# Optimization experiments

Measured on AMD Instinct MI355X. Metric: run time of the kernel, lower is better.

The kernel has to match this reference:

```python
import jax, jax.numpy as jnp
import numpy as np

LN_EPS = 1e-6
NEG = -1e9

def setup_inputs() -> dict:
    key = jax.random.key(0)
    k1, k2, k3 = jax.random.split(key, 3)
    B, S, E, H = 4, 2048, 1024, 4
    D = E // H
    x = jax.random.normal(k1, (B, S, E), dtype=jnp.float32)
    qkv_w = jax.random.normal(k2, (3, H, E, D), dtype=jnp.float32) * 0.02
    out_w = jax.random.normal(k3, (E, E), dtype=jnp.float32) * 0.02
    ln_gamma = jnp.ones((E,), dtype=jnp.float32)
    ln_beta = jnp.zeros((E,), dtype=jnp.float32)
    return {"x": x, "qkv_w": qkv_w, "out_w": out_w, "ln_gamma": ln_gamma, "ln_beta": ln_beta}

def reference(x, qkv_w, out_w, ln_gamma, ln_beta):
    B, S, E = x.shape
    H = qkv_w.shape[1]
    q = jnp.einsum('bse,hed->bhsd', x, qkv_w[0])
    k = jnp.einsum('bse,hed->bhsd', x, qkv_w[1])
    v = jnp.einsum('bse,hed->bhsd', x, qkv_w[2])
    # NOTE: original scales by sqrt(embedding_size), NOT sqrt(head_dim).
    scores = jnp.einsum('bhsd,bhtd->bhst', q, k) / jnp.sqrt(jnp.float32(E))
    # look-ahead (causal) mask: 1 above diagonal -> add -1e9
    causal = 1.0 - jnp.tril(jnp.ones((S, S), dtype=scores.dtype))
    scores = scores + causal * NEG
    attn = jax.nn.softmax(scores, axis=-1)
    out = jnp.einsum('bhst,bhtd->bhsd', attn, v)        # [b,h,s,d]
    # concat heads -> [b,s,e]
    out = out.transpose(0, 2, 1, 3).reshape(B, S, E)
    out = out @ out_w
    y = out + x  # residual
    mean = jnp.mean(y, axis=-1, keepdims=True)
    var = jnp.mean(jnp.square(y - mean), axis=-1, keepdims=True)
    return (y - mean) * jax.lax.rsqrt(var + LN_EPS) * ln_gamma + ln_beta
```

## Files before the change

### kernel.cpp

```cpp
#include <hip/hip_runtime.h>

typedef __attribute__((ext_vector_type(8))) __bf16 bf16x8;
typedef __attribute__((ext_vector_type(4))) float f32x4;
typedef __attribute__((ext_vector_type(16))) float f32x16;
typedef unsigned short u16;
typedef unsigned int u32;

#define BB 4
#define SS 2048
#define EE 1024
#define HH 4
#define DD 256

#define GLOAD_LDS(g, l) __builtin_amdgcn_global_load_lds( \
    (const __attribute__((address_space(1))) unsigned int*)(g), \
    (__attribute__((address_space(3))) unsigned int*)(l), 16, 0, 0)

__device__ __forceinline__ u16 f2bf(float f) {
  unsigned int u = __float_as_uint(f);
  u = (u + 0x7FFFu + ((u >> 16) & 1u)) >> 16;
  return (u16)u;
}

__global__ __launch_bounds__(256) void cast_bf16_k(const float* __restrict__ in,
                                                   u16* __restrict__ out, int n4) {
  int i = blockIdx.x * 256 + threadIdx.x;
  if (i >= n4) return;
  float4 v = ((const float4*)in)[i];
  union { u16 s[4]; uint2 u; } o;
  o.s[0] = f2bf(v.x); o.s[1] = f2bf(v.y); o.s[2] = f2bf(v.z); o.s[3] = f2bf(v.w);
  ((uint2*)out)[i] = o.u;
}

__global__ __launch_bounds__(256) void transpose_cast_k(const float* __restrict__ in,
                                                        u16* __restrict__ out, int R, int C,
                                                        float scale_q) {
  __shared__ float tile[32][33];
  size_t moff = (size_t)blockIdx.z * R * C;
  in += moff; out += moff;
  float sc = (blockIdx.z < 4) ? scale_q : 1.0f;
  int c0 = blockIdx.x * 32, r0 = blockIdx.y * 32;
  int tx = threadIdx.x, ty = threadIdx.y;
  #pragma unroll
  for (int i = 0; i < 4; ++i)
    tile[ty + 8*i][tx] = in[(size_t)(r0 + ty + 8*i) * C + c0 + tx];
  __syncthreads();
  #pragma unroll
  for (int i = 0; i < 4; ++i)
    out[(size_t)(c0 + ty + 8*i) * R + r0 + tx] = f2bf(tile[tx][ty + 8*i] * sc);
}

__device__ __forceinline__ void gemm128(const u16* __restrict__ A, int lda,
                                        const u16* __restrict__ Bt, int ldb,
                                        int row0, int col0, int K,
                                        u16* As, u16* Bs, f32x4 acc[4][4]) {
  int t = threadIdx.x;
  int lane = t & 63, w = t >> 6;
  int wr = w >> 1, wc = w & 1;
  int lr = lane & 15, kg = lane >> 4;
  f32x4 z = {0.f, 0.f, 0.f, 0.f};
  #pragma unroll
  for (int m = 0; m < 4; ++m)
    #pragma unroll
    for (int n = 0; n < 4; ++n) acc[m][n] = z;
  for (int kt = 0; kt < K; kt += 64) {
    __syncthreads();
    #pragma unroll
    for (int it = 0; it < 4; ++it) {
      int Lb = it*4096 + w*1024 + lane*16;
      int row = Lb >> 7;
      int scb = ((Lb >> 4) & 7) ^ (row & 7);
      GLOAD_LDS(A  + (size_t)(row0 + row) * lda + kt + scb*8,
                (char*)As + it*4096 + w*1024);
      GLOAD_LDS(Bt + (size_t)(col0 + row) * ldb + kt + scb*8,
                (char*)Bs + it*4096 + w*1024);
    }
    __syncthreads();
    __builtin_amdgcn_s_setprio(1);
    #pragma unroll
    for (int kk = 0; kk < 2; ++kk) {
      bf16x8 af[4], bfr[4];
      #pragma unroll
      for (int m = 0; m < 4; ++m) {
        int row = wr*64 + m*16 + lr;
        int bo = (row << 7) + ((((kk << 6) + (kg << 4))) ^ ((row & 7) << 4));
        af[m] = *(const bf16x8*)((const char*)As + bo);
      }
      #pragma unroll
      for (int n = 0; n < 4; ++n) {
        int row = wc*64 + n*16 + lr;
        int bo = (row << 7) + ((((kk << 6) + (kg << 4))) ^ ((row & 7) << 4));
        bfr[n] = *(const bf16x8*)((const char*)Bs + bo);
      }
      #pragma unroll
      for (int m = 0; m < 4; ++m)
        #pragma unroll
        for (int n = 0; n < 4; ++n)
          acc[m][n] = __builtin_amdgcn_mfma_f32_16x16x32_bf16(af[m], bfr[n], acc[m][n], 0, 0, 0);
    }
    __builtin_amdgcn_s_setprio(0);
  }
}

__global__ __launch_bounds__(256) void qkv_gemm_k(const u16* __restrict__ xb,
                                                  const u16* __restrict__ wt,
                                                  u16* __restrict__ qb,
                                                  u16* __restrict__ kp,
                                                  u16* __restrict__ vp) {
  __shared__ u16 As[128*64], Bs[128*64];
  int bid = blockIdx.x;
  int mh = bid >> 7;
  int tt = bid & 127;
  int mt = tt & 63, nt = tt >> 6;
  f32x4 acc[4][4];
  gemm128(xb, EE, wt + (size_t)mh * DD * EE, EE, mt*128, nt*128, EE, As, Bs, acc);
  int t = threadIdx.x, lane = t & 63, w = t >> 6;
  int wr = w >> 1, wc = w & 1, lr = lane & 15, kg = lane >> 4;
  int qi = mh >> 2, h = mh & 3;
  if (qi == 0) {
    #pragma unroll
    for (int m = 0; m < 4; ++m)
      #pragma unroll
      for (int n = 0; n < 4; ++n)
        #pragma unroll
        for (int j = 0; j < 4; ++j) {
          int r = mt*128 + wr*64 + m*16 + kg*4 + j;
          int c = nt*128 + wc*64 + n*16 + lr;
          int b = r >> 11, s = r & 2047;
          qb[(size_t)((b*HH + h) * SS + s) * DD + c] = f2bf(acc[m][n][j]);
        }
  } else if (qi == 1) {
    #pragma unroll
    for (int m = 0; m < 4; ++m)
      #pragma unroll
      for (int n = 0; n < 4; ++n)
        #pragma unroll
        for (int j = 0; j < 4; ++j) {
          int r = mt*128 + wr*64 + m*16 + kg*4 + j;
          int d = nt*128 + wc*64 + n*16 + lr;
          int b = r >> 11, srow = r & 2047;
          int bh = b*HH + h, c = srow >> 5, l31 = srow & 31;
          int kb = d >> 4, hfd = (d >> 3) & 1, e = d & 7;
          kp[(((size_t)(bh*64 + c)*16 + kb)*64 + hfd*32 + l31)*8 + e] = f2bf(acc[m][n][j]);
        }
  } else {
    int hfs = (kg >> 1) & 1, e0 = (kg & 1) * 4;
    #pragma unroll
    for (int m = 0; m < 4; ++m)
      #pragma unroll
      for (int n = 0; n < 4; ++n) {
        int r = mt*128 + wr*64 + m*16 + kg*4;
        int d = nt*128 + wc*64 + n*16 + lr;
        int b = r >> 11, srow = r & 2047;
        int bh = b*HH + h, c = srow >> 5;
        int kb2 = (srow >> 4) & 1;
        int db = d >> 5, l31 = d & 31;
        union { u16 s4[4]; uint2 u; } pk;
        #pragma unroll
        for (int j = 0; j < 4; ++j) pk.s4[j] = f2bf(acc[m][n][j]);
        *(uint2*)(vp + ((((size_t)(bh*64 + c)*8 + db)*2 + kb2)*64 + hfs*32 + l31)*8 + e0) = pk.u;
      }
  }
}

__global__ __launch_bounds__(512, 2) void attn_k(const u16* __restrict__ Qb,
                                                 const u16* __restrict__ Kp,
                                                 const u16* __restrict__ Vp,
                                                 u16* __restrict__ ctx) {
  int bid = blockIdx.x;
  int xcd = bid & 7;
  int p   = bid >> 3;
  int tid = threadIdx.x, wid = tid >> 6, lane = tid & 63;
  int ks = wid & 3, dh = wid >> 2;
  int l31 = lane & 31, hf = lane >> 5;

  __shared__ float Ob[32 * 256];
  __shared__ float stats[4][32][2];
  __shared__ u16 Qs[16 * 64 * 8];

  for (int bhp = 0; bhp < 2; ++bhp) {
    int bh = xcd + 8 * bhp;
    int b = bh >> 2, h = bh & 3;
    const u16* Q = Qb + (size_t)bh * SS * DD;
    size_t bh64 = (size_t)bh * 64;

    for (int tp = 0; tp < 2; ++tp) {
      int qt = tp ? p : 63 - p;
      int q0 = qt * 32;

      #pragma unroll
      for (int i = 0; i < 2; ++i) {
        int kb = wid*2 + i;
        uint4 qv = *(const uint4*)(Q + (size_t)(q0 + l31) * DD + kb*16 + hf*8);
        *(uint4*)((char*)Qs + kb*1024 + lane*16) = qv;
      }
      __syncthreads();

      f32x16 o[4];
      #pragma unroll
      for (int j = 0; j < 4; ++j)
        #pragma unroll
        for (int r = 0; r < 16; ++r) o[j][r] = 0.f;
      float m = -1e30f, lsum = 0.f;

      int n = qt + 1;
      int c0 = (n * ks) >> 2, c1 = (n * (ks + 1)) >> 2;

      for (int c = c0; c < c1; ++c) {
        const u16* kpc = Kp + (bh64 + c) * (16 * 512);
        const u16* vpc = Vp + (bh64 + c) * (16 * 512);
        bf16x8 vf[8];
        #pragma unroll
        for (int i = 0; i < 8; ++i)
          vf[i] = *(const bf16x8*)(vpc + (dh*8 + i)*512 + lane*8);
        bf16x8 kfa[8];
        #pragma unroll
        for (int kb = 0; kb < 8; ++kb)
          kfa[kb] = *(const bf16x8*)(kpc + kb*512 + lane*8);
        __builtin_amdgcn_sched_barrier(0);

        f32x16 sA, sB;
        #pragma unroll
        for (int r = 0; r < 16; ++r) { sA[r] = 0.f; sB[r] = 0.f; }
        __builtin_amdgcn_s_setprio(1);
        #pragma unroll
        for (int kb = 0; kb < 8; ++kb) {
          bf16x8 qv = *(const bf16x8*)((const char*)Qs + kb*1024 + lane*16);
          sA = __builtin_amdgcn_mfma_f32_32x32x16_bf16(kfa[kb], qv, sA, 0, 0, 0);
          if (kb == 3) __builtin_amdgcn_sched_barrier(0);
        }
        __builtin_amdgcn_s_setprio(0);
        __builtin_amdgcn_sched_barrier(0);
        bf16x8 kfb[8];
        #pragma unroll
        for (int kb = 0; kb < 8; ++kb)
          kfb[kb] = *(const bf16x8*)(kpc + (8 + kb)*512 + lane*8);
        __builtin_amdgcn_sched_barrier(0);
        __builtin_amdgcn_s_setprio(1);
        #pragma unroll
        for (int kb = 0; kb < 8; ++kb) {
          bf16x8 qv = *(const bf16x8*)((const char*)Qs + (8 + kb)*1024 + lane*16);
          sB = __builtin_amdgcn_mfma_f32_32x32x16_bf16(kfb[kb], qv, sB, 0, 0, 0);
          if (kb == 3) __builtin_amdgcn_sched_barrier(0);
        }
        __builtin_amdgcn_s_setprio(0);

        float pr[16];
        #pragma unroll
        for (int r = 0; r < 16; ++r) pr[r] = sA[r] + sB[r];
        if (c == qt) {
          #pragma unroll
          for (int r = 0; r < 16; ++r) {
            int key = (r & 3) + 8*(r >> 2) + 4*hf;
            if (key > l31) pr[r] = -1e9f;
          }
        }
        float mx = pr[0];
        #pragma unroll
        for (int r = 1; r < 16; ++r) mx = fmaxf(mx, pr[r]);
        mx = fmaxf(mx, __shfl_xor(mx, 32));
        if (!__all(mx <= m + 11.5f)) {
          float mnew = fmaxf(m, mx);
          float al = exp2f(m - mnew);
          lsum *= al;
          #pragma unroll
          for (int j = 0; j < 4; ++j) o[j] *= al;
          m = mnew;
        }
        float psum = 0.f;
        #pragma unroll
        for (int r = 0; r < 16; ++r) { pr[r] = exp2f(pr[r] - m); psum += pr[r]; }
        psum += __shfl_xor(psum, 32);
        lsum += psum;
        u32 cpk[8];
        #pragma unroll
        for (int i = 0; i < 8; ++i) {
          u32 rpk;
          asm("v_cvt_pk_bf16_f32 %0, %1, %2" : "=v"(rpk) : "v"(pr[2*i]), "v"(pr[2*i+1]));
          cpk[i] = rpk;
        }
        u32 x0 = (u32)__shfl_xor((int)(hf ? cpk[0] : cpk[2]), 32);
        u32 x1 = (u32)__shfl_xor((int)(hf ? cpk[1] : cpk[3]), 32);
        u32 x2 = (u32)__shfl_xor((int)(hf ? cpk[4] : cpk[6]), 32);
        u32 x3 = (u32)__shfl_xor((int)(hf ? cpk[5] : cpk[7]), 32);
        union { u32 w[4]; bf16x8 v; } pb0, pb1;
        pb0.w[0] = hf ? x0 : cpk[0];
        pb0.w[1] = hf ? x1 : cpk[1];
        pb0.w[2] = hf ? cpk[2] : x0;
        pb0.w[3] = hf ? cpk[3] : x1;
        pb1.w[0] = hf ? x2 : cpk[4];
        pb1.w[1] = hf ? x3 : cpk[5];
        pb1.w[2] = hf ? cpk[6] : x2;
        pb1.w[3] = hf ? cpk[7] : x3;
        __builtin_amdgcn_s_setprio(1);
        #pragma unroll
        for (int j = 0; j < 4; ++j) {
          o[j] = __builtin_amdgcn_mfma_f32_32x32x16_bf16(vf[j*2+0], pb0.v, o[j], 0, 0, 0);
          o[j] = __builtin_amdgcn_mfma_f32_32x32x16_bf16(vf[j*2+1], pb1.v, o[j], 0, 0, 0);
        }
        __builtin_amdgcn_s_setprio(0);
      }

      __syncthreads();
      if (lane < 32 && wid < 4) { stats[wid][l31][0] = m; stats[wid][l31][1] = lsum; }
      __syncthreads();
      float mg = fmaxf(fmaxf(stats[0][l31][0], stats[1][l31][0]),
                       fmaxf(stats[2][l31][0], stats[3][l31][0]));
      float beta = exp2f(m - mg);
      #pragma unroll
      for (int j = 0; j < 4; ++j) o[j] *= beta;

      #pragma unroll
      for (int tau = 0; tau < 4; ++tau) {
        int jr = (ks + tau) & 3;
        f32x16 osel = (jr == 0) ? o[0] : (jr == 1) ? o[1] : (jr == 2) ? o[2] : o[3];
        #pragma unroll
        for (int u = 0; u < 4; ++u) {
          int byteoff = l31*1024 + ((((dh*4 + jr)*128) + u*32 + hf*16) ^ ((l31 & 7) << 4));
          float* ptr = (float*)((char*)Ob + byteoff);
          f32x4 val = { osel[4*u+0], osel[4*u+1], osel[4*u+2], osel[4*u+3] };
          if (tau == 0) *(f32x4*)ptr = val;
          else {
            f32x4 old = *(f32x4*)ptr;
            *(f32x4*)ptr = old + val;
          }
        }
        __syncthreads();
      }

      if (tid < 256) {
        int q = tid >> 3, dg = tid & 7;
        float mgq = fmaxf(fmaxf(stats[0][q][0], stats[1][q][0]),
                          fmaxf(stats[2][q][0], stats[3][q][0]));
        float lg = exp2f(stats[0][q][0] - mgq) * stats[0][q][1]
                 + exp2f(stats[1][q][0] - mgq) * stats[1][q][1]
                 + exp2f(stats[2][q][0] - mgq) * stats[2][q][1]
                 + exp2f(stats[3][q][0] - mgq) * stats[3][q][1];
        float linv = 1.f / lg;
        u16* crow = ctx + (size_t)(b*SS + q0 + q) * EE + h*DD + dg*32;
        union { u16 s16[16]; uint4 u4[2]; } outp;
        #pragma unroll
        for (int i = 0; i < 8; ++i) {
          int byteoff = q*1024 + ((dg*128 + i*16) ^ ((q & 7) << 4));
          f32x4 v = *(const f32x4*)((const char*)Ob + byteoff);
          #pragma unroll
          for (int j = 0; j < 4; ++j) outp.s16[(i*4+j) & 15] = f2bf(v[j] * linv);
          if (i == 3) {
            *(uint4*)(crow + 0) = outp.u4[0];
            *(uint4*)(crow + 8) = outp.u4[1];
          }
          if (i == 7) {
            *(uint4*)(crow + 16) = outp.u4[0];
            *(uint4*)(crow + 24) = outp.u4[1];
          }
        }
      }
      __syncthreads();
    }
  }
}

__global__ __launch_bounds__(256) void proj_gemm_k(const u16* __restrict__ ctx,
                                                   const u16* __restrict__ wot,
                                                   const float* __restrict__ x,
                                                   float* __restrict__ y) {
  __shared__ u16 As[128*64], Bs[128*64];
  int bid = blockIdx.x;
  int mt = bid & 63, nt = bid >> 6;
  f32x4 acc[4][4];
  gemm128(ctx, EE, wot, EE, mt*128, nt*128, EE, As, Bs, acc);
  int t = threadIdx.x, lane = t & 63, w = t >> 6;
  int wr = w >> 1, wc = w & 1, lr = lane & 15, kg = lane >> 4;
  #pragma unroll
  for (int m = 0; m < 4; ++m)
    #pragma unroll
    for (int n = 0; n < 4; ++n)
      #pragma unroll
      for (int j = 0; j < 4; ++j) {
        int r = mt*128 + wr*64 + m*16 + kg*4 + j;
        int c = nt*128 + wc*64 + n*16 + lr;
        size_t idx = (size_t)r * EE + c;
        y[idx] = acc[m][n][j] + x[idx];
      }
}

__global__ __launch_bounds__(256) void ln_k(float* __restrict__ y,
                                            const float* __restrict__ gamma,
                                            const float* __restrict__ beta) {
  int row = blockIdx.x;
  int t = threadIdx.x;
  float4 v = *((const float4*)(y + (size_t)row * EE) + t);
  float s = v.x + v.y + v.z + v.w;
  float ss = v.x*v.x + v.y*v.y + v.z*v.z + v.w*v.w;
  #pragma unroll
  for (int off = 1; off < 64; off <<= 1) {
    s  += __shfl_xor(s, off);
    ss += __shfl_xor(ss, off);
  }
  __shared__ float rs[4], rss[4];
  int w = t >> 6, lane = t & 63;
  if (lane == 0) { rs[w] = s; rss[w] = ss; }
  __syncthreads();
  s  = rs[0] + rs[1] + rs[2] + rs[3];
  ss = rss[0] + rss[1] + rss[2] + rss[3];
  float mean = s * (1.f / EE);
  float var  = ss * (1.f / EE) - mean * mean;
  float rstd = rsqrtf(var + 1e-6f);
  float4 g  = *((const float4*)gamma + t);
  float4 be = *((const float4*)beta + t);
  float4 ov;
  ov.x = (v.x - mean) * rstd * g.x + be.x;
  ov.y = (v.y - mean) * rstd * g.y + be.y;
  ov.z = (v.z - mean) * rstd * g.z + be.z;
  ov.w = (v.w - mean) * rstd * g.w + be.w;
  *((float4*)(y + (size_t)row * EE) + t) = ov;
}

extern "C" void kernel_launch(void* const* d_in, const int* in_sizes, int n_in,
                              void* d_out, int out_size, void* d_ws, size_t ws_size,
                              hipStream_t stream) {
  const float* x      = (const float*)d_in[0];
  const float* qkv_w  = (const float*)d_in[1];
  const float* out_w  = (const float*)d_in[2];
  const float* gamma  = (const float*)d_in[3];
  const float* beta   = (const float*)d_in[4];
  float* out = (float*)d_out;
  char* ws = (char*)d_ws;

  u16* xb  = (u16*)(ws);
  u16* ctx = xb;
  u16* wqt = (u16*)(ws + 16777216);
  u16* wot = (u16*)(ws + 23068672);
  u16* Qb  = (u16*)(ws + 25165824);
  u16* Kpb = Qb + (size_t)BB*HH*SS*DD;
  u16* Vpb = Kpb + (size_t)BB*HH*SS*DD;

  const float QSC = 0.03125f * 1.44269504088896340736f;

  cast_bf16_k<<<8192, 256, 0, stream>>>(x, xb, (BB*SS*EE)/4);
  transpose_cast_k<<<dim3(8, 32, 12), dim3(32, 8), 0, stream>>>(qkv_w, wqt, EE, DD, QSC);
  transpose_cast_k<<<dim3(32, 32, 1), dim3(32, 8), 0, stream>>>(out_w, wot, EE, EE, 1.0f);
  qkv_gemm_k<<<1536, 256, 0, stream>>>(xb, wqt, Qb, Kpb, Vpb);
  attn_k<<<256, 512, 0, stream>>>(Qb, Kpb, Vpb, ctx);
  proj_gemm_k<<<512, 256, 0, stream>>>(ctx, wot, x, out);
  ln_k<<<8192, 256, 0, stream>>>(out, gamma, beta);
}
```

Before: 202.0 us.

## Double-buffer K/V register fragments to prefetch next attention chunk

Measured after the change: 304.3 us. 50.6% more time.

```diff
diff --git a/kernel.cpp b/kernel.cpp
--- a/kernel.cpp
+++ b/kernel.cpp
@@ -155,12 +155,115 @@
         int bh = b*HH + h, c = srow >> 5;
         int kb2 = (srow >> 4) & 1;
         int db = d >> 5, l31 = d & 31;
-        union { u16 s4[4]; uint2 u; } pk;
+        union { u16 s4[4]; uint2 u2; } pk;
         #pragma unroll
         for (int j = 0; j < 4; ++j) pk.s4[j] = f2bf(acc[m][n][j]);
-        *(uint2*)(vp + ((((size_t)(bh*64 + c)*8 + db)*2 + kb2)*64 + hfs*32 + l31)*8 + e0) = pk.u;
-      }
-  }
+        *(uint2*)(vp + ((((size_t)(bh*64 + c)*8 + db)*2 + kb2)*64 + hfs*32 + l31)*8 + e0) = pk.u2;
+      }
+  }
+}
+
+__device__ __forceinline__ void attn_chunk(
+    int c, int qt, int c1,
+    const u16* __restrict__ Kp0, const u16* __restrict__ Vp0,
+    int dh, int l31, int hf, int lane, const char* Qs,
+    bf16x8 (&kc)[8], bf16x8 (&vc)[8],
+    bf16x8 (&kn)[8], bf16x8 (&vn)[8],
+    f32x16 (&o)[4], float& m, float& lsum) {
+  const u16* kpc = Kp0 + (size_t)c * (16 * 512);
+  bf16x8 kfb[8];
+  #pragma unroll
+  for (int kb = 0; kb < 8; ++kb)
+    kfb[kb] = *(const bf16x8*)(kpc + (8 + kb)*512 + lane*8);
+  __builtin_amdgcn_sched_barrier(0);
+
+  f32x16 sA, sB;
+  #pragma unroll
+  for (int r = 0; r < 16; ++r) { sA[r] = 0.f; sB[r] = 0.f; }
+  __builtin_amdgcn_s_setprio(1);
+  #pragma unroll
+  for (int kb = 0; kb < 8; ++kb) {
+    bf16x8 qv = *(const bf16x8*)(Qs + kb*1024 + lane*16);
+    sA = __builtin_amdgcn_mfma_f32_32x32x16_bf16(kc[kb], qv, sA, 0, 0, 0);
+    if (kb == 3) __builtin_amdgcn_sched_barrier(0);
+  }
+  __builtin_amdgcn_s_setprio(0);
+  __builtin_amdgcn_sched_barrier(0);
+  __builtin_amdgcn_s_setprio(1);
+  #pragma unroll
+  for (int kb = 0; kb < 8; ++kb) {
+    bf16x8 qv = *(const bf16x8*)(Qs + (8 + kb)*1024 + lane*16);
+    sB = __builtin_amdgcn_mfma_f32_32x32x16_bf16(kfb[kb], qv, sB, 0, 0, 0);
+    if (kb == 3) __builtin_amdgcn_sched_barrier(0);
+  }
+  __builtin_amdgcn_s_setprio(0);
+
+  float pr[16];
+  #pragma unroll
+  for (int r = 0; r < 16; ++r) pr[r] = sA[r] + sB[r];
+  if (c == qt) {
+    #pragma unroll
+    for (int r = 0; r < 16; ++r) {
+      int key = (r & 3) + 8*(r >> 2) + 4*hf;
+      if (key > l31) pr[r] = -1e9f;
+    }
+  }
+  float mx = pr[0];
+  #pragma unroll
+  for (int r = 1; r < 16; ++r) mx = fmaxf(mx, pr[r]);
+  mx = fmaxf(mx, __shfl_xor(mx, 32));
+  if (!__all(mx <= m + 11.5f)) {
+    float mnew = fmaxf(m, mx);
+    float al = exp2f(m - mnew);
+    lsum *= al;
+    #pragma unroll
+    for (int j = 0; j < 4; ++j) o[j] *= al;
+    m = mnew;
+  }
+  float psum = 0.f;
+  #pragma unroll
+  for (int r = 0; r < 16; ++r) { pr[r] = exp2f(pr[r] - m); psum += pr[r]; }
+  psum += __shfl_xor(psum, 32);
+  lsum += psum;
+
+  if (c + 1 < c1) {
+    const u16* kpn = Kp0 + (size_t)(c + 1) * (16 * 512);
+    const u16* vpn = Vp0 + (size_t)(c + 1) * (16 * 512);
+    #pragma unroll
+    for (int i = 0; i < 8; ++i)
+      vn[i] = *(const bf16x8*)(vpn + (dh*8 + i)*512 + lane*8);
+    #pragma unroll
+    for (int kb = 0; kb < 8; ++kb)
+      kn[kb] = *(const bf16x8*)(kpn + kb*512 + lane*8);
+  }
+
+  u32 cpk[8];
+  #pragma unroll
+  for (int i = 0; i < 8; ++i) {
+    u32 rpk;
+    asm("v_cvt_pk_bf16_f32 %0, %1, %2" : "=v"(rpk) : "v"(pr[2*i]), "v"(pr[2*i+1]));
+    cpk[i] = rpk;
+  }
+  u32 x0 = (u32)__shfl_xor((int)(hf ? cpk[0] : cpk[2]), 32);
+  u32 x1 = (u32)__shfl_xor((int)(hf ? cpk[1] : cpk[3]), 32);
+  u32 x2 = (u32)__shfl_xor((int)(hf ? cpk[4] : cpk[6]), 32);
+  u32 x3 = (u32)__shfl_xor((int)(hf ? cpk[5] : cpk[7]), 32);
+  union { u32 w[4]; bf16x8 v; } pb0, pb1;
+  pb0.w[0] = hf ? x0 : cpk[0];
+  pb0.w[1] = hf ? x1 : cpk[1];
+  pb0.w[2] = hf ? cpk[2] : x0;
+  pb0.w[3] = hf ? cpk[3] : x1;
+  pb1.w[0] = hf ? x2 : cpk[4];
+  pb1.w[1] = hf ? x3 : cpk[5];
+  pb1.w[2] = hf ? cpk[6] : x2;
+  pb1.w[3] = hf ? cpk[7] : x3;
+  __builtin_amdgcn_s_setprio(1);
+  #pragma unroll
+  for (int j = 0; j < 4; ++j) {
+    o[j] = __builtin_amdgcn_mfma_f32_32x32x16_bf16(vc[j*2+0], pb0.v, o[j], 0, 0, 0);
+    o[j] = __builtin_amdgcn_mfma_f32_32x32x16_bf16(vc[j*2+1], pb1.v, o[j], 0, 0, 0);
+  }
+  __builtin_amdgcn_s_setprio(0);
 }
 
 __global__ __launch_bounds__(512, 2) void attn_k(const u16* __restrict__ Qb,
@@ -182,7 +285,8 @@
     int bh = xcd + 8 * bhp;
     int b = bh >> 2, h = bh & 3;
     const u16* Q = Qb + (size_t)bh * SS * DD;
-    size_t bh64 = (size_t)bh * 64;
+    const u16* Kp0 = Kp + (size_t)bh * 64 * (16 * 512);
+    const u16* Vp0 = Vp + (size_t)bh * 64 * (16 * 512);
 
     for (int tp = 0; tp < 2; ++tp) {
       int qt = tp ? p : 63 - p;
@@ -206,99 +310,27 @@
       int n = qt + 1;
       int c0 = (n * ks) >> 2, c1 = (n * (ks + 1)) >> 2;
 
-      for (int c = c0; c < c1; ++c) {
-        const u16* kpc = Kp + (bh64 + c) * (16 * 512);
-        const u16* vpc = Vp + (bh64 + c) * (16 * 512);
-        bf16x8 vf[8];
-        #pragma unroll
-        for (int i = 0; i < 8; ++i)
-          vf[i] = *(const bf16x8*)(vpc + (dh*8 + i)*512 + lane*8);
-        bf16x8 kfa[8];
-        #pragma unroll
-        for (int kb = 0; kb < 8; ++kb)
-          kfa[kb] = *(const bf16x8*)(kpc + kb*512 + lane*8);
-        __builtin_amdgcn_sched_barrier(0);
-
-        f32x16 sA, sB;
-        #pragma unroll
-        for (int r = 0; r < 16; ++r) { sA[r] = 0.f; sB[r] = 0.f; }
-        __builtin_amdgcn_s_setprio(1);
-        #pragma unroll
-        for (int kb = 0; kb < 8; ++kb) {
-          bf16x8 qv = *(const bf16x8*)((const char*)Qs + kb*1024 + lane*16);
-          sA = __builtin_amdgcn_mfma_f32_32x32x16_bf16(kfa[kb], qv, sA, 0, 0, 0);
-          if (kb == 3) __builtin_amdgcn_sched_barrier(0);
-        }
-        __builtin_amdgcn_s_setprio(0);
-        __builtin_amdgcn_sched_barrier(0);
-        bf16x8 kfb[8];
-        #pragma unroll
-        for (int kb = 0; kb < 8; ++kb)
-          kfb[kb] = *(const bf16x8*)(kpc + (8 + kb)*512 + lane*8);
-        __builtin_amdgcn_sched_barrier(0);
-        __builtin_amdgcn_s_setprio(1);
-        #pragma unroll
-        for (int kb = 0; kb < 8; ++kb) {
-          bf16x8 qv = *(const bf16x8*)((const char*)Qs + (8 + kb)*1024 + lane*16);
-          sB = __builtin_amdgcn_mfma_f32_32x32x16_bf16(kfb[kb], qv, sB, 0, 0, 0);
-          if (kb == 3) __builtin_amdgcn_sched_barrier(0);
-        }
-        __builtin_amdgcn_s_setprio(0);
-
-        float pr[16];
-        #pragma unroll
-        for (int r = 0; r < 16; ++r) pr[r] = sA[r] + sB[r];
-        if (c == qt) {
+      if (c0 < c1) {
+        bf16x8 kA[8], vA[8], kB[8], vB[8];
+        {
+          const u16* kpc = Kp0 + (size_t)c0 * (16 * 512);
+          const u16* vpc = Vp0 + (size_t)c0 * (16 * 512);
           #pragma unroll
-          for (int r = 0; r < 16; ++r) {
-            int key = (r & 3) + 8*(r >> 2) + 4*hf;
-            if (key > l31) pr[r] = -1e9f;
-          }
-        }
-        float mx = pr[0];
-        #pragma unroll
-        for (int r = 1; r < 16; ++r) mx = fmaxf(mx, pr[r]);
-        mx = fmaxf(mx, __shfl_xor(mx, 32));
-        if (!__all(mx <= m + 11.5f)) {
-          float mnew = fmaxf(m, mx);
-          float al = exp2f(m - mnew);
-          lsum *= al;
+          for (int i = 0; i < 8; ++i)
+            vA[i] = *(const bf16x8*)(vpc + (dh*8 + i)*512 + lane*8);
           #pragma unroll
-          for (int j = 0; j < 4; ++j) o[j] *= al;
-          m = mnew;
-        }
-        float psum = 0.f;
-        #pragma unroll
-        for (int r = 0; r < 16; ++r) { pr[r] = exp2f(pr[r] - m); psum += pr[r]; }
-        psum += __shfl_xor(psum, 32);
-        lsum += psum;
-        u32 cpk[8];
-        #pragma unroll
-        for (int i = 0; i < 8; ++i) {
-          u32 rpk;
-          asm("v_cvt_pk_bf16_f32 %0, %1, %2" : "=v"(rpk) : "v"(pr[2*i]), "v"(pr[2*i+1]));
-          cpk[i] = rpk;
-        }
-        u32 x0 = (u32)__shfl_xor((int)(hf ? cpk[0] : cpk[2]), 32);
-        u32 x1 = (u32)__shfl_xor((int)(hf ? cpk[1] : cpk[3]), 32);
-        u32 x2 = (u32)__shfl_xor((int)(hf ? cpk[4] : cpk[6]), 32);
-        u32 x3 = (u32)__shfl_xor((int)(hf ? cpk[5] : cpk[7]), 32);
-        union { u32 w[4]; bf16x8 v; } pb0, pb1;
-        pb0.w[0] = hf ? x0 : cpk[0];
-        pb0.w[1] = hf ? x1 : cpk[1];
-        pb0.w[2] = hf ? cpk[2] : x0;
-        pb0.w[3] = hf ? cpk[3] : x1;
-        pb1.w[0] = hf ? x2 : cpk[4];
-        pb1.w[1] = hf ? x3 : cpk[5];
-        pb1.w[2] = hf ? cpk[6] : x2;
-        pb1.w[3] = hf ? cpk[7] : x3;
-        __builtin_amdgcn_s_setprio(1);
-        #pragma unroll
-        for (int j = 0; j < 4; ++j) {
-          o[j] = __builtin_amdgcn_mfma_f32_32x32x16_bf16(vf[j*2+0], pb0.v, o[j], 0, 0, 0);
-          o[j] = __builtin_amdgcn_mfma_f32_32x32x16_bf16(vf[j*2+1], pb1.v, o[j], 0, 0, 0);
-        }
-        __builtin_amdgcn_s_setprio(0);
+          for (int kb = 0; kb < 8; ++kb)
+            kA[kb] = *(const bf16x8*)(kpc + kb*512 + lane*8);
+        }
+        int c = c0;
+        while (true) {
+          attn_chunk(c, qt, c1, Kp0, Vp0, dh, l31, hf, lane,
+                     (const char*)Qs, kA, vA, kB, vB, o, m, lsum);
+          if (++c >= c1) break;
+          attn_chunk(c, qt, c1, Kp0, Vp0, dh, l31, hf, lane,
+                     (const char*)Qs, kB, vB, kA, vA, o, m, lsum);
+          if (++c >= c1) break;
+        }
       }
 
       __syncthreads();
```
